# Performance work log

Hardware: AMD Instinct MI355X
Metric: run time of the kernel (lower is better)

## Reference

```python
import jax, jax.numpy as jnp
import numpy as np

H = 64
VOCAB = 64
NUM_PAIRS = 6
ENERGY_THRESHOLD = 0.4
LN_EPS = 1e-5


def setup_inputs() -> dict:
    key = jax.random.key(0)
    ks = jax.random.split(key, 16)
    B, L = 256, 2048
    s = 0.05
    return {
        "x": jax.random.randint(ks[0], (B, L), 0, VOCAB),
        "embed": jax.random.normal(ks[1], (VOCAB, H), jnp.float32) * s,
        "W1": jax.random.normal(ks[2], (2 * H, H), jnp.float32) * s,
        "b1": jnp.zeros((2 * H,), jnp.float32),
        "W2": jax.random.normal(ks[3], (H, 2 * H), jnp.float32) * s,
        "b2": jnp.zeros((H,), jnp.float32),
        "ln_g": jnp.ones((H,), jnp.float32),
        "ln_b": jnp.zeros((H,), jnp.float32),
        "Wk": jax.random.normal(ks[4], (H, H), jnp.float32) * s,
        "Wv": jax.random.normal(ks[5], (H, H), jnp.float32) * s,
        "Wq": jax.random.normal(ks[6], (H, H), jnp.float32) * s,
        "Wr": jax.random.normal(ks[7], (H, H), jnp.float32) * s,
        "alpha": jnp.float32(0.5),
        "Wout": jax.random.normal(ks[8], (VOCAB, H), jnp.float32) * s,
        "bout": jnp.zeros((VOCAB,), jnp.float32),
    }


def _layernorm(x, g, b):
    mu = jnp.mean(x, axis=-1, keepdims=True)
    var = jnp.var(x, axis=-1, keepdims=True)
    return (x - mu) * jax.lax.rsqrt(var + LN_EPS) * g + b


def _encoder(x, embed, W1, b1, W2, b2, ln_g, ln_b):
    h = embed[x]                                  # [B, L, H]
    ff = jax.nn.relu(h @ W1.T + b1) @ W2.T + b2   # [B, L, H]
    return _layernorm(h + ff, ln_g, ln_b)


def _forward(x, embed, W1, b1, W2, b2, ln_g, ln_b, Wk, Wv, Wq, Wr, alpha, Wout, bout):
    h = _encoder(x, embed, W1, b1, W2, b2, ln_g, ln_b)  # [B, L, H]
    B, L, _ = h.shape

    def step(M, h_t):  # M: [B, H, H], h_t: [B, H]
        k = h_t @ Wk.T
        k = k / jnp.maximum(jnp.linalg.norm(k, axis=-1, keepdims=True), 1e-12)
        v = h_t @ Wv.T
        pred = jnp.einsum("bij,bj->bi", M, k)
        delta = v - pred
        gate = (jnp.linalg.norm(delta, axis=-1) >
                ENERGY_THRESHOLD * jnp.linalg.norm(v, axis=-1)).astype(M.dtype)
        M = M + gate[:, None, None] * delta[:, :, None] * k[:, None, :]
        return M, None

    M0 = jnp.zeros((B, H, H), h.dtype)
    M, _ = jax.lax.scan(step, M0, jnp.swapaxes(h, 0, 1))  # scan over L

    q = h[:, -1, :] @ Wq.T                 # [B, H]
    slots = jnp.swapaxes(M, 1, 2)          # [B, H, H]
    k_s = min(NUM_PAIRS + 2, H)
    norms = jnp.linalg.norm(slots, axis=-1)            # [B, H]
    _, topk_i = jax.lax.top_k(norms, k_s)              # [B, k_s]
    sel = jnp.take_along_axis(slots, topk_i[:, :, None], axis=1)  # [B, k_s, H]
    q_r = q @ Wr.T
    attn = jax.nn.softmax(jnp.einsum("bkh,bh->bk", sel, q_r) / jnp.sqrt(jnp.float32(H)), axis=-1)
    retro_ctx = jnp.einsum("bk,bkh->bh", attn, sel)    # [B, H]
    m_ctx = jnp.einsum("bij,bj->bi", M, q)             # [B, H]
    a = jax.nn.sigmoid(alpha)
    mixed = jax.nn.relu(a * retro_ctx + (1.0 - a) * m_ctx)
    return mixed @ Wout.T + bout           # [B, VOCAB]


def reference(x, embed, W1, b1, W2, b2, ln_g, ln_b, Wk, Wv, Wq, Wr, alpha, Wout, bout):
    return _forward(x, embed, W1, b1, W2, b2, ln_g, ln_b, Wk, Wv, Wq, Wr, alpha, Wout, bout)
```

## Files before the change

kernel.cpp:

```cpp
#include <hip/hip_runtime.h>
#include <math.h>

#define H 64
#define VOCABN 64
#define LSEQ 2048
#define LN_EPS 1e-5f

template <int CTRL>
__device__ __forceinline__ float dpp_add(float x) {
  return x + __int_as_float(__builtin_amdgcn_update_dpp(
      0, __float_as_int(x), CTRL, 0xF, 0xF, true));
}

__device__ __forceinline__ float wave_allsum(float x) {
  x = dpp_add<0xB1>(x);
  x = dpp_add<0x4E>(x);
  x = dpp_add<0x141>(x);
  x = dpp_add<0x140>(x);
  x += __shfl_xor(x, 16, 64);
  x += __shfl_xor(x, 32, 64);
  return x;
}

__device__ __forceinline__ float reduce_to_lane63(float x) {
  x = dpp_add<0x111>(x);
  x = dpp_add<0x112>(x);
  x = dpp_add<0x114>(x);
  x = dpp_add<0x118>(x);
  x = dpp_add<0x142>(x);
  x = dpp_add<0x143>(x);
  return x;
}

__global__ __launch_bounds__(64) void tables_kernel(
    const float* __restrict__ embed, const float* __restrict__ W1, const float* __restrict__ b1,
    const float* __restrict__ W2, const float* __restrict__ b2,
    const float* __restrict__ ln_g, const float* __restrict__ ln_b,
    const float* __restrict__ Wk, const float* __restrict__ Wv,
    float* __restrict__ Htab, float* __restrict__ Ktab, float* __restrict__ Vtab,
    float* __restrict__ nvtab)
{
  __shared__ float hs[H];
  __shared__ float ff1[2 * H];
  __shared__ float lns[H];
  const int c = blockIdx.x;
  const int i = threadIdx.x;

  float e = embed[c * H + i];
  hs[i] = e;
  __syncthreads();

  float r1 = b1[i], r2 = b1[i + H];
  for (int j = 0; j < H; ++j) {
    float hj = hs[j];
    r1 = fmaf(W1[i * H + j], hj, r1);
    r2 = fmaf(W1[(i + H) * H + j], hj, r2);
  }
  ff1[i]     = fmaxf(r1, 0.f);
  ff1[i + H] = fmaxf(r2, 0.f);
  __syncthreads();

  float o = b2[i];
  for (int m = 0; m < 2 * H; ++m) o = fmaf(W2[i * 2 * H + m], ff1[m], o);
  float y = e + o;

  float mu  = wave_allsum(y) * (1.f / H);
  float d   = y - mu;
  float var = wave_allsum(d * d) * (1.f / H);
  float ln  = d * (1.f / sqrtf(var + LN_EPS)) * ln_g[i] + ln_b[i];
  lns[i] = ln;
  __syncthreads();
  Htab[c * H + i] = ln;

  float k = 0.f, v = 0.f;
  for (int j = 0; j < H; ++j) {
    float lj = lns[j];
    k = fmaf(Wk[i * H + j], lj, k);
    v = fmaf(Wv[i * H + j], lj, v);
  }
  float nk = sqrtf(wave_allsum(k * k));
  Ktab[c * H + i] = k / fmaxf(nk, 1e-12f);
  Vtab[c * H + i] = v;
  float nv = sqrtf(wave_allsum(v * v));
  if (i == 0) nvtab[c] = 0.4f * nv;
}

__global__ __launch_bounds__(256, 1) void scan_kernel(
    const int* __restrict__ x, const float* __restrict__ Htab,
    const float* __restrict__ Ktab, const float* __restrict__ Vtab,
    const float* __restrict__ nvtab,
    const float* __restrict__ Wq, const float* __restrict__ Wr,
    const float* __restrict__ alpha, const float* __restrict__ Wout,
    const float* __restrict__ bout, float* __restrict__ out)
{
  __shared__ float4 Kl4[VOCABN * H / 4];
  __shared__ float4 Vl4[VOCABN * H / 4];
  __shared__ float4 Gl4[VOCABN * H / 4];
  __shared__ float4 Rl4[VOCABN * H / 4];
  __shared__ int4   xl4[LSEQ / 4];
  __shared__ float  thl[VOCABN];
  __shared__ float  hbuf[H];
  __shared__ float  qbuf[H];
  __shared__ float  mbuf[H];
  float* Kl = (float*)Kl4;
  float* Vl = (float*)Vl4;
  float* Gl = (float*)Gl4;
  float* Rl = (float*)Rl4;
  int*   xl = (int*)xl4;

  const int b    = blockIdx.x;
  const int tid  = threadIdx.x;
  const int lane = tid & 63;
  const int wid  = tid >> 6;

  {
    const float4* Kg = (const float4*)Ktab;
    const float4* Vg = (const float4*)Vtab;
    for (int q = tid; q < VOCABN * H / 4; q += 256) {
      float4 vq = Vg[q];
      Kl4[q] = Kg[q]; Vl4[q] = vq; Rl4[q] = vq;
    }
    const int4* xg = (const int4*)(x + b * LSEQ);
    for (int q = tid; q < LSEQ / 4; q += 256) xl4[q] = xg[q];
    if (tid < VOCABN) thl[tid] = nvtab[tid];
  }
  __syncthreads();

  {
    float4 kr[16];
#pragma unroll
    for (int q = 0; q < 16; ++q) kr[q] = Kl4[lane * 16 + q];
    for (int r = 0; r < 16; ++r) {
      const int c2 = wid * 16 + r;
      const float4* kp2 = (const float4*)(Kl + c2 * H);
      float a0 = 0.f, a1 = 0.f, a2 = 0.f, a3 = 0.f;
#pragma unroll
      for (int q = 0; q < 16; ++q) {
        float4 kq = kp2[q];
        a0 = fmaf(kr[q].x, kq.x, a0);
        a1 = fmaf(kr[q].y, kq.y, a1);
        a2 = fmaf(kr[q].z, kq.z, a2);
        a3 = fmaf(kr[q].w, kq.w, a3);
      }
      Gl[c2 * H + lane] = (a0 + a1) + (a2 + a3);
    }
  }
  __syncthreads();

  float4 Mw[4];
#pragma unroll
  for (int q = 0; q < 4; ++q) Mw[q] = make_float4(0.f, 0.f, 0.f, 0.f);

  int   c0 = xl[0], c1 = xl[1];
  float rv  = Rl[c0 * H + lane];
  float rvn = Rl[c1 * H + lane];
  float th0 = thl[c0], th1 = thl[c1];

  for (int t = 0; t < LSEQ; ++t) {
    const int ix2 = (t + 2 < LSEQ) ? t + 2 : LSEQ - 1;
    const int c2  = xl[ix2];
    float rb2  = Rl[c2 * H + lane];
    float th2v = thl[c2];
    float g01  = Gl[c0 * H + c1];
    float g02  = Gl[c0 * H + c2];

    float nd2 = reduce_to_lane63(rv * rv);
    float nds = sqrtf(__int_as_float(__builtin_amdgcn_readlane(__float_as_int(nd2), 63)));
    float thu = __int_as_float(__builtin_amdgcn_readfirstlane(__float_as_int(th0)));

    if (nds > thu) {
      const float delta = rv;
      rvn = fmaf(-g01, delta, rvn);
      rb2 = fmaf(-g02, delta, rb2);
      __syncthreads();
      const float4* gp = ((const float4*)(Gl + c0 * H)) + wid * 4;
      float4 ga = gp[0], gb = gp[1], gc = gp[2], gd = gp[3];
      float gs[16] = {ga.x, ga.y, ga.z, ga.w, gb.x, gb.y, gb.z, gb.w,
                      gc.x, gc.y, gc.z, gc.w, gd.x, gd.y, gd.z, gd.w};
#pragma unroll
      for (int r = 0; r < 16; ++r) {
        const int cc = wid * 16 + r;
        Rl[cc * H + lane] = fmaf(-gs[r], delta, Rl[cc * H + lane]);
      }
      const float4* kp = ((const float4*)(Kl + c0 * H)) + wid * 4;
#pragma unroll
      for (int q = 0; q < 4; ++q) {
        float4 k4 = kp[q];
        Mw[q].x = fmaf(delta, k4.x, Mw[q].x);
        Mw[q].y = fmaf(delta, k4.y, Mw[q].y);
        Mw[q].z = fmaf(delta, k4.z, Mw[q].z);
        Mw[q].w = fmaf(delta, k4.w, Mw[q].w);
      }
      __syncthreads();
    }
    rv = rvn; rvn = rb2; c0 = c1; c1 = c2; th0 = th1; th1 = th2v;
  }

  __syncthreads();
#pragma unroll
  for (int r = 0; r < 4; ++r) {
    const int jb = wid * 16 + r * 4;
    float4 m = Mw[r];
    Vl[(jb + 0) * H + lane] = m.x;
    Vl[(jb + 1) * H + lane] = m.y;
    Vl[(jb + 2) * H + lane] = m.z;
    Vl[(jb + 3) * H + lane] = m.w;
    Kl[lane * H + jb + 0] = m.x;
    Kl[lane * H + jb + 1] = m.y;
    Kl[lane * H + jb + 2] = m.z;
    Kl[lane * H + jb + 3] = m.w;
  }
  __syncthreads();

  if (wid == 0) {
    const int clast = xl[LSEQ - 1];
    hbuf[lane] = Htab[clast * H + lane];

    float qi = 0.f;
    for (int j = 0; j < H; ++j) qi = fmaf(Wq[lane * H + j], hbuf[j], qi);
    qbuf[lane] = qi;

    float qri = 0.f;
    for (int j = 0; j < H; ++j) qri = fmaf(Wr[lane * H + j], qbuf[j], qri);

    float n2 = 0.f;
    for (int i2 = 0; i2 < H; ++i2) { float m = Kl[i2 * H + lane]; n2 = fmaf(m, m, n2); }

    const int KS = 8;
    int idxs[KS];
    float nloc = n2;
#pragma unroll
    for (int k = 0; k < KS; ++k) {
      float v = nloc; int idx = lane;
#pragma unroll
      for (int s = 1; s < 64; s <<= 1) {
        float ov = __shfl_xor(v, s, 64);
        int   oi = __shfl_xor(idx, s, 64);
        if (ov > v || (ov == v && oi < idx)) { v = ov; idx = oi; }
      }
      idxs[k] = idx;
      if (lane == idx) nloc = -1.f;
    }

    float sel[KS], lg[KS];
#pragma unroll
    for (int k = 0; k < KS; ++k) {
      float s = Vl[idxs[k] * H + lane];
      sel[k] = s;
      lg[k] = wave_allsum(s * qri) * 0.125f;
    }
    float lmax = lg[0];
#pragma unroll
    for (int k = 1; k < KS; ++k) lmax = fmaxf(lmax, lg[k]);
    float esum = 0.f, retro = 0.f;
#pragma unroll
    for (int k = 0; k < KS; ++k) {
      float e = expf(lg[k] - lmax);
      esum += e;
      retro = fmaf(e, sel[k], retro);
    }
    retro /= esum;

    float mc = 0.f;
    for (int j = 0; j < H; ++j) mc = fmaf(Vl[j * H + lane], qbuf[j], mc);

    float a = 1.f / (1.f + expf(-alpha[0]));
    float mixed = fmaxf(fmaf(a, retro, (1.f - a) * mc), 0.f);
    mbuf[lane] = mixed;

    float oo = bout[lane];
    for (int i2 = 0; i2 < H; ++i2) oo = fmaf(Wout[lane * H + i2], mbuf[i2], oo);
    out[b * VOCABN + lane] = oo;
  }
}

extern "C" void kernel_launch(void* const* d_in, const int* in_sizes, int n_in,
                              void* d_out, int out_size, void* d_ws, size_t ws_size,
                              hipStream_t stream) {
  const int*   x     = (const int*)d_in[0];
  const float* embed = (const float*)d_in[1];
  const float* W1    = (const float*)d_in[2];
  const float* b1    = (const float*)d_in[3];
  const float* W2    = (const float*)d_in[4];
  const float* b2    = (const float*)d_in[5];
  const float* ln_g  = (const float*)d_in[6];
  const float* ln_b  = (const float*)d_in[7];
  const float* Wk    = (const float*)d_in[8];
  const float* Wv    = (const float*)d_in[9];
  const float* Wq    = (const float*)d_in[10];
  const float* Wr    = (const float*)d_in[11];
  const float* alpha = (const float*)d_in[12];
  const float* Wout  = (const float*)d_in[13];
  const float* bout  = (const float*)d_in[14];
  float* out = (float*)d_out;

  const int B = in_sizes[0] / LSEQ;

  float* ws    = (float*)d_ws;
  float* Htab  = ws;
  float* Ktab  = ws + 4096;
  float* Vtab  = ws + 8192;
  float* nvtab = ws + 12288;

  tables_kernel<<<VOCABN, 64, 0, stream>>>(embed, W1, b1, W2, b2, ln_g, ln_b,
                                           Wk, Wv, Htab, Ktab, Vtab, nvtab);
  scan_kernel<<<B, 256, 0, stream>>>(x, Htab, Ktab, Vtab, nvtab,
                                     Wq, Wr, alpha, Wout, bout, out);
}
```

Baseline: 561.9 us.

## Batch scan steps into chunks of eight with precomputed pairwise Gram coefficients

Restructures the sequential delta-rule scan so each chunk of 8 tokens first resolves gates and residual corrections within the chunk using precomputed pairwise Gram entries, then applies a single rank-8 update to the shared residual table and memory registers. This replaces up to two block barriers per token with two per chunk and amortizes LDS traffic over 8 updates. A prepass fills a per-chunk table of 28 Gram coefficients, and the V copy in shared memory is dropped, with the Gram buffer reused for the final M. The cost is more register pressure and redundant per-wave gate computation.

```diff
diff --git a/kernel.cpp b/kernel.cpp
--- a/kernel.cpp
+++ b/kernel.cpp
@@ -5,6 +5,8 @@
 #define VOCABN 64
 #define LSEQ 2048
 #define LN_EPS 1e-5f
+#define TCH 8
+#define NCHUNK (LSEQ / TCH)
 
 template <int CTRL>
 __device__ __forceinline__ float dpp_add(float x) {
@@ -30,6 +32,10 @@
   x = dpp_add<0x142>(x);
   x = dpp_add<0x143>(x);
   return x;
+}
+
+__device__ __forceinline__ float rdlf(float v, int lane) {
+  return __int_as_float(__builtin_amdgcn_readlane(__float_as_int(v), lane));
 }
 
 __global__ __launch_bounds__(64) void tables_kernel(
@@ -94,19 +100,16 @@
     const float* __restrict__ bout, float* __restrict__ out)
 {
   __shared__ float4 Kl4[VOCABN * H / 4];
-  __shared__ float4 Vl4[VOCABN * H / 4];
-  __shared__ float4 Gl4[VOCABN * H / 4];
+  __shared__ float  Gl[VOCABN * H];
   __shared__ float4 Rl4[VOCABN * H / 4];
-  __shared__ int4   xl4[LSEQ / 4];
+  __shared__ int    xl[LSEQ];
+  __shared__ float4 gin4[NCHUNK * 8];
   __shared__ float  thl[VOCABN];
   __shared__ float  hbuf[H];
   __shared__ float  qbuf[H];
   __shared__ float  mbuf[H];
   float* Kl = (float*)Kl4;
-  float* Vl = (float*)Vl4;
-  float* Gl = (float*)Gl4;
   float* Rl = (float*)Rl4;
-  int*   xl = (int*)xl4;
 
   const int b    = blockIdx.x;
   const int tid  = threadIdx.x;
@@ -116,11 +119,9 @@
   {
     const float4* Kg = (const float4*)Ktab;
     const float4* Vg = (const float4*)Vtab;
-    for (int q = tid; q < VOCABN * H / 4; q += 256) {
-      float4 vq = Vg[q];
-      Kl4[q] = Kg[q]; Vl4[q] = vq; Rl4[q] = vq;
-    }
+    for (int q = tid; q < VOCABN * H / 4; q += 256) { Kl4[q] = Kg[q]; Rl4[q] = Vg[q]; }
     const int4* xg = (const int4*)(x + b * LSEQ);
+    int4* xl4 = (int4*)xl;
     for (int q = tid; q < LSEQ / 4; q += 256) xl4[q] = xg[q];
     if (tid < VOCABN) thl[tid] = nvtab[tid];
   }
@@ -147,64 +148,113 @@
   }
   __syncthreads();
 
+  for (int n = tid; n < NCHUNK; n += 256) {
+    const int base = n * TCH;
+    int ct[8];
+#pragma unroll
+    for (int i = 0; i < 8; ++i) ct[i] = xl[base + i];
+    float* gout = (float*)(gin4 + n * 8);
+    int idx = 0;
+    for (int i = 0; i < 7; ++i)
+      for (int j = i + 1; j < 8; ++j)
+        gout[idx++] = Gl[ct[i] * H + ct[j]];
+  }
+  __syncthreads();
+
   float4 Mw[4];
 #pragma unroll
   for (int q = 0; q < 4; ++q) Mw[q] = make_float4(0.f, 0.f, 0.f, 0.f);
 
-  int   c0 = xl[0], c1 = xl[1];
-  float rv  = Rl[c0 * H + lane];
-  float rvn = Rl[c1 * H + lane];
-  float th0 = thl[c0], th1 = thl[c1];
-
-  for (int t = 0; t < LSEQ; ++t) {
-    const int ix2 = (t + 2 < LSEQ) ? t + 2 : LSEQ - 1;
-    const int c2  = xl[ix2];
-    float rb2  = Rl[c2 * H + lane];
-    float th2v = thl[c2];
-    float g01  = Gl[c0 * H + c1];
-    float g02  = Gl[c0 * H + c2];
-
-    float nd2 = reduce_to_lane63(rv * rv);
-    float nds = sqrtf(__int_as_float(__builtin_amdgcn_readlane(__float_as_int(nd2), 63)));
-    float thu = __int_as_float(__builtin_amdgcn_readfirstlane(__float_as_int(th0)));
-
-    if (nds > thu) {
-      const float delta = rv;
-      rvn = fmaf(-g01, delta, rvn);
-      rb2 = fmaf(-g02, delta, rb2);
-      __syncthreads();
-      const float4* gp = ((const float4*)(Gl + c0 * H)) + wid * 4;
-      float4 ga = gp[0], gb = gp[1], gc = gp[2], gd = gp[3];
-      float gs[16] = {ga.x, ga.y, ga.z, ga.w, gb.x, gb.y, gb.z, gb.w,
-                      gc.x, gc.y, gc.z, gc.w, gd.x, gd.y, gd.z, gd.w};
-#pragma unroll
-      for (int r = 0; r < 16; ++r) {
-        const int cc = wid * 16 + r;
-        Rl[cc * H + lane] = fmaf(-gs[r], delta, Rl[cc * H + lane]);
-      }
-      const float4* kp = ((const float4*)(Kl + c0 * H)) + wid * 4;
-#pragma unroll
-      for (int q = 0; q < 4; ++q) {
-        float4 k4 = kp[q];
-        Mw[q].x = fmaf(delta, k4.x, Mw[q].x);
-        Mw[q].y = fmaf(delta, k4.y, Mw[q].y);
-        Mw[q].z = fmaf(delta, k4.z, Mw[q].z);
-        Mw[q].w = fmaf(delta, k4.w, Mw[q].w);
-      }
-      __syncthreads();
-    }
-    rv = rvn; rvn = rb2; c0 = c1; c1 = c2; th0 = th1; th1 = th2v;
-  }
-
-  __syncthreads();
+  for (int n = 0; n < NCHUNK; ++n) {
+    const int base = n * TCH;
+    const int4 t0 = *(const int4*)(xl + base);
+    const int4 t1 = *(const int4*)(xl + base + 4);
+    int c_[8];
+    c_[0] = __builtin_amdgcn_readfirstlane(t0.x);
+    c_[1] = __builtin_amdgcn_readfirstlane(t0.y);
+    c_[2] = __builtin_amdgcn_readfirstlane(t0.z);
+    c_[3] = __builtin_amdgcn_readfirstlane(t0.w);
+    c_[4] = __builtin_amdgcn_readfirstlane(t1.x);
+    c_[5] = __builtin_amdgcn_readfirstlane(t1.y);
+    c_[6] = __builtin_amdgcn_readfirstlane(t1.z);
+    c_[7] = __builtin_amdgcn_readfirstlane(t1.w);
+
+    float rr[8], tt[8], dd[8];
+#pragma unroll
+    for (int i = 0; i < 8; ++i) { rr[i] = Rl[c_[i] * H + lane]; tt[i] = thl[c_[i]]; }
+
+    float gg[28];
+    {
+      float4 gq[7];
+#pragma unroll
+      for (int k = 0; k < 7; ++k) gq[k] = gin4[n * 8 + k];
+#pragma unroll
+      for (int k = 0; k < 28; ++k)
+        gg[k] = (k % 4 == 0) ? gq[k / 4].x : (k % 4 == 1) ? gq[k / 4].y
+              : (k % 4 == 2) ? gq[k / 4].z : gq[k / 4].w;
+    }
+
+#pragma unroll
+    for (int i = 0; i < 8; ++i) {
+      float nd2 = reduce_to_lane63(rr[i] * rr[i]);
+      float nds = sqrtf(rdlf(nd2, 63));
+      float thu = __int_as_float(__builtin_amdgcn_readfirstlane(__float_as_int(tt[i])));
+      dd[i] = 0.f;
+      if (nds > thu) {
+        dd[i] = rr[i];
+#pragma unroll
+        for (int j = i + 1; j < 8; ++j)
+          rr[j] = fmaf(-gg[i * (15 - i) / 2 + (j - i - 1)], dd[i], rr[j]);
+      }
+    }
+
+    __syncthreads();
+#pragma unroll
+    for (int g = 0; g < 4; ++g) {
+      float4 Gq[8];
+#pragma unroll
+      for (int i = 0; i < 8; ++i)
+        Gq[i] = ((const float4*)(Gl + c_[i] * H))[wid * 4 + g];
+#pragma unroll
+      for (int r = 0; r < 4; ++r) {
+        const int cc = wid * 16 + g * 4 + r;
+        float val = Rl[cc * H + lane];
+#pragma unroll
+        for (int i = 0; i < 8; ++i) {
+          const float co = (r == 0) ? Gq[i].x : (r == 1) ? Gq[i].y
+                         : (r == 2) ? Gq[i].z : Gq[i].w;
+          val = fmaf(-co, dd[i], val);
+        }
+        Rl[cc * H + lane] = val;
+      }
+    }
+#pragma unroll
+    for (int q = 0; q < 4; ++q) {
+      float4 Kq[8];
+#pragma unroll
+      for (int i = 0; i < 8; ++i)
+        Kq[i] = ((const float4*)(Kl + c_[i] * H))[wid * 4 + q];
+#pragma unroll
+      for (int i = 0; i < 8; ++i) {
+        Mw[q].x = fmaf(dd[i], Kq[i].x, Mw[q].x);
+        Mw[q].y = fmaf(dd[i], Kq[i].y, Mw[q].y);
+        Mw[q].z = fmaf(dd[i], Kq[i].z, Mw[q].z);
+        Mw[q].w = fmaf(dd[i], Kq[i].w, Mw[q].w);
+      }
+    }
+    __syncthreads();
+  }
+
+  __syncthreads();
+  float* Mt = Gl;
 #pragma unroll
   for (int r = 0; r < 4; ++r) {
     const int jb = wid * 16 + r * 4;
     float4 m = Mw[r];
-    Vl[(jb + 0) * H + lane] = m.x;
-    Vl[(jb + 1) * H + lane] = m.y;
-    Vl[(jb + 2) * H + lane] = m.z;
-    Vl[(jb + 3) * H + lane] = m.w;
+    Mt[(jb + 0) * H + lane] = m.x;
+    Mt[(jb + 1) * H + lane] = m.y;
+    Mt[(jb + 2) * H + lane] = m.z;
+    Mt[(jb + 3) * H + lane] = m.w;
     Kl[lane * H + jb + 0] = m.x;
     Kl[lane * H + jb + 1] = m.y;
     Kl[lane * H + jb + 2] = m.z;
@@ -223,12 +273,12 @@
     float qri = 0.f;
     for (int j = 0; j < H; ++j) qri = fmaf(Wr[lane * H + j], qbuf[j], qri);
 
-    float n2 = 0.f;
-    for (int i2 = 0; i2 < H; ++i2) { float m = Kl[i2 * H + lane]; n2 = fmaf(m, m, n2); }
+    float n2r = 0.f;
+    for (int i2 = 0; i2 < H; ++i2) { float m = Kl[i2 * H + lane]; n2r = fmaf(m, m, n2r); }
 
     const int KS = 8;
     int idxs[KS];
-    float nloc = n2;
+    float nloc = n2r;
 #pragma unroll
     for (int k = 0; k < KS; ++k) {
       float v = nloc; int idx = lane;
@@ -245,7 +295,7 @@
     float sel[KS], lg[KS];
 #pragma unroll
     for (int k = 0; k < KS; ++k) {
-      float s = Vl[idxs[k] * H + lane];
+      float s = Mt[idxs[k] * H + lane];
       sel[k] = s;
       lg[k] = wave_allsum(s * qri) * 0.125f;
     }
@@ -262,7 +312,7 @@
     retro /= esum;
 
     float mc = 0.f;
-    for (int j = 0; j < H; ++j) mc = fmaf(Vl[j * H + lane], qbuf[j], mc);
+    for (int j = 0; j < H; ++j) mc = fmaf(Mt[j * H + lane], qbuf[j], mc);
 
     float a = 1.f / (1.f + expf(-alpha[0]));
     float mixed = fmaxf(fmaf(a, retro, (1.f - a) * mc), 0.f);
```

Result: no change. 567.8 us (+1.0%).
